# Optimization experiments

Measured on AMD Instinct MI355X. Metric: run time of the kernel, lower is better.

## Reference

```python
import jax, jax.numpy as jnp
import numpy as np

BLOCK = 64
N_HEADS = 16
HEAD_DIM = 64
HIDDEN = N_HEADS * HEAD_DIM
W_BLOCKS = 3   # sliding window blocks (centered: i-1, i, i+1)
G_BLOCKS = 1   # global blocks (block 0)
LN_EPS = 1e-12
NEG = -1e9


def _build_layout(nblk):
    """Static bigbird-style block layout: per query block, indices of attended key blocks.
    Returns idx [nblk, G+W] int32 and valid [nblk, G+W] bool (dedup'd, range-checked)."""
    nkb = G_BLOCKS + W_BLOCKS
    idx = np.zeros((nblk, nkb), dtype=np.int32)
    valid = np.zeros((nblk, nkb), dtype=bool)
    globals_ = list(range(G_BLOCKS))
    half = W_BLOCKS // 2
    for i in range(nblk):
        cands = globals_ + [i - half + j for j in range(W_BLOCKS)]
        seen = set()
        for c, cand in enumerate(cands):
            ok = (0 <= cand < nblk) and (cand not in seen)
            if ok:
                seen.add(cand)
            idx[i, c] = min(max(cand, 0), nblk - 1)
            valid[i, c] = ok
    return jnp.asarray(idx), jnp.asarray(valid)


def setup_inputs() -> dict:
    key = jax.random.key(0)
    ks = jax.random.split(key, 8)
    b, s = 4, 4096
    sd = 1.0 / np.sqrt(HIDDEN)
    inp = {
        "hidden_states": jax.random.normal(ks[0], (b, s, HIDDEN), dtype=jnp.float32),
        "attention_mask": jnp.zeros((b, s), dtype=jnp.float32),
        "wq": jax.random.normal(ks[1], (HIDDEN, HIDDEN), dtype=jnp.float32) * sd,
        "bq": jnp.zeros((HIDDEN,), dtype=jnp.float32),
        "wk": jax.random.normal(ks[2], (HIDDEN, HIDDEN), dtype=jnp.float32) * sd,
        "bk": jnp.zeros((HIDDEN,), dtype=jnp.float32),
        "wv": jax.random.normal(ks[3], (HIDDEN, HIDDEN), dtype=jnp.float32) * sd,
        "bv": jnp.zeros((HIDDEN,), dtype=jnp.float32),
        "wo": jax.random.normal(ks[4], (HIDDEN, HIDDEN), dtype=jnp.float32) * sd,
        "bo": jnp.zeros((HIDDEN,), dtype=jnp.float32),
        "ln_g": jnp.ones((HIDDEN,), dtype=jnp.float32),
        "ln_b": jnp.zeros((HIDDEN,), dtype=jnp.float32),
    }
    return inp


def _sparse_attention(hidden_states, attention_mask, wq, bq, wk, bk, wv, bv, wo, bo, ln_g, ln_b):
    b, s, h = hidden_states.shape
    nblk = s // BLOCK
    idx, valid = _build_layout(nblk)          # [nblk, nkb]
    nkb = idx.shape[1]

    def proj(w, bias):
        y = hidden_states @ w.T + bias                      # [b, s, H]
        return y.reshape(b, s, N_HEADS, HEAD_DIM).transpose(0, 2, 1, 3)  # [b, h, s, d]

    q = proj(wq, bq)
    k = proj(wk, bk)
    v = proj(wv, bv)

    # blockify: [b, h, nblk, BLOCK, d]
    qb = q.reshape(b, N_HEADS, nblk, BLOCK, HEAD_DIM)
    kb = k.reshape(b, N_HEADS, nblk, BLOCK, HEAD_DIM)
    vb = v.reshape(b, N_HEADS, nblk, BLOCK, HEAD_DIM)

    # gather attended key/value blocks per query block: [b, h, nblk, nkb, BLOCK, d]
    kg = kb[:, :, idx]
    vg = vb[:, :, idx]

    scale = 1.0 / np.sqrt(HEAD_DIM)
    # scores: [b, h, nblk, BLOCK(q), nkb, BLOCK(k)]
    scores = jnp.einsum("bhnqd,bhnmkd->bhnqmk", qb, kg) * scale

    # key padding mask (additive float), gathered to sparse layout
    kp = attention_mask.reshape(b, nblk, BLOCK)[:, idx]      # [b, nblk, nkb, BLOCK]
    scores = scores + kp[:, None, :, None, :, :]
    # invalid (out-of-layout) blocks
    scores = jnp.where(valid[None, None, :, None, :, None], scores, NEG)

    # softmax over all attended keys (nkb * BLOCK)
    flat = scores.reshape(b, N_HEADS, nblk, BLOCK, nkb * BLOCK)
    probs = jax.nn.softmax(flat, axis=-1).reshape(scores.shape)

    ctx = jnp.einsum("bhnqmk,bhnmkd->bhnqd", probs, vg)      # [b, h, nblk, BLOCK, d]
    ctx = ctx.reshape(b, N_HEADS, s, HEAD_DIM).transpose(0, 2, 1, 3).reshape(b, s, h)

    # output projection + residual + LayerNorm (dropout in eval mode = identity)
    y = ctx @ wo.T + bo + hidden_states
    mu = jnp.mean(y, axis=-1, keepdims=True)
    var = jnp.mean((y - mu) ** 2, axis=-1, keepdims=True)
    return (y - mu) * jax.lax.rsqrt(var + LN_EPS) * ln_g + ln_b


def reference(hidden_states, attention_mask, wq, bq, wk, bk, wv, bv, wo, bo, ln_g, ln_b):
    return _sparse_attention(hidden_states, attention_mask, wq, bq, wk, bk, wv, bv, wo, bo, ln_g, ln_b)
```

## Files before the change

kernel.cpp:

```cpp
#include <hip/hip_runtime.h>
#include <cstdint>
#include <cstddef>


using f32x4 = __attribute__((ext_vector_type(4))) float;
using s16x8 = __attribute__((ext_vector_type(8))) short;
using u16x4 = __attribute__((ext_vector_type(4))) unsigned short;

#define NEGV -1000000000.0f

__device__ __forceinline__ unsigned short f2b(float f) {
  unsigned u = __float_as_uint(f);
  u += 0x7FFFu + ((u >> 16) & 1u);
  return (unsigned short)(u >> 16);
}

#define GLDS(g, l)                                                        \
  __builtin_amdgcn_global_load_lds(                                       \
      (__attribute__((address_space(1))) void*)(g),                       \
      (__attribute__((address_space(3))) void*)(l), 16, 0, 0)

__global__ __launch_bounds__(256) void cast_hidden(const float* __restrict__ in,
                                                   unsigned short* __restrict__ out) {
  size_t i = (size_t)blockIdx.x * 256 + threadIdx.x;
  float4 v = ((const float4*)in)[i];
  u16x4 o = {f2b(v.x), f2b(v.y), f2b(v.z), f2b(v.w)};
  ((u16x4*)out)[i] = o;
}

__global__ __launch_bounds__(256) void cast_weights(const float* __restrict__ w0,
                                                    const float* __restrict__ w1,
                                                    const float* __restrict__ w2,
                                                    const float* __restrict__ w3,
                                                    unsigned short* __restrict__ out) {
  const float* src = blockIdx.y == 0 ? w0 : blockIdx.y == 1 ? w1 : blockIdx.y == 2 ? w2 : w3;
  size_t i = (size_t)blockIdx.x * 256 + threadIdx.x;
  float4 v = ((const float4*)src)[i];
  u16x4 o = {f2b(v.x), f2b(v.y), f2b(v.z), f2b(v.w)};
  ((u16x4*)(out + (size_t)blockIdx.y * 1048576))[i] = o;
}

template <int MODE>
__global__ __launch_bounds__(256) void gemm128(const unsigned short* __restrict__ A,
                                               const unsigned short* __restrict__ B,
                                               const float* __restrict__ bias,
                                               const float* __restrict__ resid,
                                               void* __restrict__ outp) {
  __shared__ __align__(16) unsigned short As[4096];
  __shared__ __align__(16) unsigned short Bs[4096];
  const int t = threadIdx.x;
  const int wave = t >> 6, lane = t & 63;
  const int quad = lane >> 4, lr = lane & 15;
  const int wm = (wave >> 1) << 6, wn = (wave & 1) << 6;
  const int bm = blockIdx.x << 7, bn = blockIdx.y << 7;

  f32x4 acc[4][4] = {};

  const int srow = t >> 2;
  const int sq = (t & 3) ^ ((srow >> 1) & 3);
  const char* Ag = (const char*)A + (((size_t)(bm + srow)) << 11) + (sq << 4);
  const char* Bg = (const char*)B + (((size_t)(bn + srow)) << 11) + (sq << 4);
  char* AsW = (char*)As + (t << 4);
  char* BsW = (char*)Bs + (t << 4);

  for (int kt = 0; kt < 2048; kt += 64) {
    __syncthreads();
    GLDS(Ag + kt, AsW);
    GLDS(Ag + kt + (64ll << 11), AsW + 4096);
    GLDS(Bg + kt, BsW);
    GLDS(Bg + kt + (64ll << 11), BsW + 4096);
    __syncthreads();
    s16x8 af[4], bf[4];
#pragma unroll
    for (int i = 0; i < 4; ++i) {
      const int ra = wm + i * 16 + lr;
      af[i] = *(const s16x8*)((const char*)As + ra * 64 + ((quad ^ ((ra >> 1) & 3)) << 4));
      const int rb = wn + i * 16 + lr;
      bf[i] = *(const s16x8*)((const char*)Bs + rb * 64 + ((quad ^ ((rb >> 1) & 3)) << 4));
    }
#pragma unroll
    for (int i = 0; i < 4; ++i)
#pragma unroll
      for (int j = 0; j < 4; ++j)
        acc[i][j] = __builtin_amdgcn_mfma_f32_16x16x32_bf16(af[i], bf[j], acc[i][j], 0, 0, 0);
  }

  float bv[4];
#pragma unroll
  for (int j = 0; j < 4; ++j) bv[j] = bias[bn + wn + j * 16 + lr];

  if (MODE == 0) {
    unsigned short* o = (unsigned short*)outp;
    int hh[4], dd[4];
#pragma unroll
    for (int j = 0; j < 4; ++j) {
      int n = bn + wn + j * 16 + lr;
      hh[j] = n >> 6;
      dd[j] = n & 63;
    }
#pragma unroll
    for (int i = 0; i < 4; ++i) {
#pragma unroll
      for (int r = 0; r < 4; ++r) {
        int m = bm + wm + i * 16 + quad * 4 + r;
        int bb = m >> 12, sl = m & 4095;
        size_t base = ((size_t)bb * 16) * 262144 + (size_t)sl * 64;
#pragma unroll
        for (int j = 0; j < 4; ++j)
          o[base + (size_t)hh[j] * 262144 + dd[j]] = f2b(acc[i][j][r] + bv[j]);
      }
    }
  } else {
    float* o = (float*)outp;
#pragma unroll
    for (int i = 0; i < 4; ++i) {
#pragma unroll
      for (int r = 0; r < 4; ++r) {
        size_t m = bm + wm + i * 16 + quad * 4 + r;
        const float* rr = resid + m * 1024 + bn + wn;
        float* orow = o + m * 1024 + bn + wn;
#pragma unroll
        for (int j = 0; j < 4; ++j)
          orow[j * 16 + lr] = acc[i][j][r] + bv[j] + rr[j * 16 + lr];
      }
    }
  }
}

__global__ __launch_bounds__(256) void attn(const unsigned short* __restrict__ Q,
                                            const unsigned short* __restrict__ K,
                                            const unsigned short* __restrict__ V,
                                            const float* __restrict__ amask,
                                            unsigned short* __restrict__ ctx) {
  __shared__ __align__(16) char smem[70656];
  char* Qs = smem;
  char* Ks = smem + 9216;
  char* Pb = smem;
  char* Vt = smem + 33792;
  float* maskL = (float*)(smem + 67584);
  float* wmaxL = (float*)(smem + 68608);
  float* wsumL = (float*)(smem + 69632);

  const int qi = blockIdx.x, h = blockIdx.y, b = blockIdx.z;
  const int t = threadIdx.x;
  const int wave = t >> 6, lane = t & 63;
  const int quad = lane >> 4, lr = lane & 15;

  int kb[4], kv[4];
  kb[0] = 0; kv[0] = 1;
#pragma unroll
  for (int c = 1; c < 4; ++c) {
    int cand = qi - 2 + c;
    kv[c] = (cand >= 1 && cand < 64);
    kb[c] = cand < 0 ? 0 : (cand > 63 ? 63 : cand);
  }

  const size_t bh = ((size_t)b * 16 + h) * 262144;
  const unsigned short* Qg = Q + bh + (size_t)qi * 4096;

  {
    int row = t >> 3, ch = t & 7;
    *(s16x8*)(Qs + row * 144 + ch * 16) = *(const s16x8*)((const char*)Qg + row * 128 + ch * 16);
    *(s16x8*)(Qs + (row + 32) * 144 + ch * 16) =
        *(const s16x8*)((const char*)Qg + (row + 32) * 128 + ch * 16);
#pragma unroll
    for (int c = 0; c < 4; ++c) {
      const unsigned short* Kg = K + bh + (size_t)kb[c] * 4096;
      char* Kc = Ks + c * 9216;
      *(s16x8*)(Kc + row * 144 + ch * 16) = *(const s16x8*)((const char*)Kg + row * 128 + ch * 16);
      *(s16x8*)(Kc + (row + 32) * 144 + ch * 16) =
          *(const s16x8*)((const char*)Kg + (row + 32) * 128 + ch * 16);
    }
  }
  {
    int c = t >> 6, kk = t & 63;
    float mv = amask[(size_t)b * 4096 + kb[c] * 64 + kk];
    maskL[c * 64 + kk] = kv[c] ? mv : mv + NEGV;
  }
  __syncthreads();

  f32x4 s[4][4] = {};
  const char* Kc = Ks + wave * 9216;
#pragma unroll
  for (int ks = 0; ks < 2; ++ks) {
    s16x8 af[4], bf[4];
#pragma unroll
    for (int i = 0; i < 4; ++i) {
      af[i] = *(const s16x8*)(Qs + (i * 16 + lr) * 144 + ks * 64 + quad * 16);
      bf[i] = *(const s16x8*)(Kc + (i * 16 + lr) * 144 + ks * 64 + quad * 16);
    }
#pragma unroll
    for (int i = 0; i < 4; ++i)
#pragma unroll
      for (int j = 0; j < 4; ++j)
        s[i][j] = __builtin_amdgcn_mfma_f32_16x16x32_bf16(af[i], bf[j], s[i][j], 0, 0, 0);
  }
#pragma unroll
  for (int j = 0; j < 4; ++j) {
    const float mj = maskL[wave * 64 + j * 16 + lr];
#pragma unroll
    for (int i = 0; i < 4; ++i)
#pragma unroll
      for (int r = 0; r < 4; ++r) s[i][j][r] = s[i][j][r] * 0.125f + mj;
  }
  __syncthreads();

#pragma unroll
  for (int i = 0; i < 4; ++i)
#pragma unroll
    for (int r = 0; r < 4; ++r) {
      float m0 = fmaxf(fmaxf(s[i][0][r], s[i][1][r]), fmaxf(s[i][2][r], s[i][3][r]));
      m0 = fmaxf(m0, __shfl_xor(m0, 1, 64));
      m0 = fmaxf(m0, __shfl_xor(m0, 2, 64));
      m0 = fmaxf(m0, __shfl_xor(m0, 4, 64));
      m0 = fmaxf(m0, __shfl_xor(m0, 8, 64));
      if (lr == 0) wmaxL[(i * 16 + quad * 4 + r) * 4 + wave] = m0;
    }

  {
    int kk = t & 63, dc0 = t >> 6;
#pragma unroll
    for (int c = 0; c < 4; ++c) {
      const unsigned short* Vg = V + bh + (size_t)kb[c] * 4096 + (size_t)kk * 64;
#pragma unroll
      for (int rr = 0; rr < 2; ++rr) {
        int dc = dc0 + rr * 4;
        s16x8 vv = *(const s16x8*)(Vg + dc * 8);
#pragma unroll
        for (int e = 0; e < 8; ++e)
          *(unsigned short*)(Vt + (dc * 8 + e) * 528 + (c * 64 + kk) * 2) = vv[e];
      }
    }
  }
  __syncthreads();

#pragma unroll
  for (int i = 0; i < 4; ++i)
#pragma unroll
    for (int r = 0; r < 4; ++r) {
      int row = i * 16 + quad * 4 + r;
      f32x4 wmv = *(const f32x4*)(wmaxL + row * 4);
      float g = fmaxf(fmaxf(wmv[0], wmv[1]), fmaxf(wmv[2], wmv[3]));
      float sm = 0.f;
#pragma unroll
      for (int j = 0; j < 4; ++j) {
        float e = __expf(s[i][j][r] - g);
        s[i][j][r] = e;
        sm += e;
      }
      sm += __shfl_xor(sm, 1, 64);
      sm += __shfl_xor(sm, 2, 64);
      sm += __shfl_xor(sm, 4, 64);
      sm += __shfl_xor(sm, 8, 64);
      if (lr == 0) wsumL[row * 4 + wave] = sm;
    }
#pragma unroll
  for (int i = 0; i < 4; ++i)
#pragma unroll
    for (int r = 0; r < 4; ++r) {
      char* prow = Pb + (i * 16 + quad * 4 + r) * 528 + wave * 128 + lr * 2;
#pragma unroll
      for (int j = 0; j < 4; ++j) *(unsigned short*)(prow + j * 32) = f2b(s[i][j][r]);
    }
  __syncthreads();

  f32x4 acc2[4] = {};
  const char* Prow = Pb + (wave * 16 + lr) * 528;
#pragma unroll
  for (int ks = 0; ks < 8; ++ks) {
    s16x8 a = *(const s16x8*)(Prow + ks * 64 + quad * 16);
#pragma unroll
    for (int j = 0; j < 4; ++j) {
      s16x8 bb2 = *(const s16x8*)(Vt + (j * 16 + lr) * 528 + ks * 64 + quad * 16);
      acc2[j] = __builtin_amdgcn_mfma_f32_16x16x32_bf16(a, bb2, acc2[j], 0, 0, 0);
    }
  }
  float inv[4];
#pragma unroll
  for (int r = 0; r < 4; ++r) {
    int row = wave * 16 + quad * 4 + r;
    f32x4 wsv = *(const f32x4*)(wsumL + row * 4);
    inv[r] = 1.0f / (wsv[0] + wsv[1] + wsv[2] + wsv[3]);
  }
#pragma unroll
  for (int r = 0; r < 4; ++r) {
    size_t srow = (size_t)qi * 64 + wave * 16 + quad * 4 + r;
    size_t base = ((size_t)b * 4096 + srow) * 1024 + h * 64;
#pragma unroll
    for (int j = 0; j < 4; ++j) ctx[base + j * 16 + lr] = f2b(acc2[j][r] * inv[r]);
  }
}

__global__ __launch_bounds__(256) void lnorm(float* __restrict__ y,
                                             const float* __restrict__ g,
                                             const float* __restrict__ bta) {
  __shared__ float red[8];
  float4* p = (float4*)(y + (size_t)blockIdx.x * 1024);
  float4 v = p[threadIdx.x];
  float s1 = v.x + v.y + v.z + v.w;
  float s2 = v.x * v.x + v.y * v.y + v.z * v.z + v.w * v.w;
#pragma unroll
  for (int m = 1; m <= 32; m <<= 1) {
    s1 += __shfl_xor(s1, m, 64);
    s2 += __shfl_xor(s2, m, 64);
  }
  int wv = threadIdx.x >> 6;
  if ((threadIdx.x & 63) == 0) {
    red[wv] = s1;
    red[4 + wv] = s2;
  }
  __syncthreads();
  float t1 = red[0] + red[1] + red[2] + red[3];
  float t2 = red[4] + red[5] + red[6] + red[7];
  float mu = t1 * (1.0f / 1024.0f);
  float var = t2 * (1.0f / 1024.0f) - mu * mu;
  float rs = rsqrtf(var + 1e-12f);
  float4 gg = ((const float4*)g)[threadIdx.x];
  float4 bb = ((const float4*)bta)[threadIdx.x];
  float4 o;
  o.x = (v.x - mu) * rs * gg.x + bb.x;
  o.y = (v.y - mu) * rs * gg.y + bb.y;
  o.z = (v.z - mu) * rs * gg.z + bb.z;
  o.w = (v.w - mu) * rs * gg.w + bb.w;
  p[threadIdx.x] = o;
}

extern "C" void kernel_launch(void* const* d_in, const int* in_sizes, int n_in,
                              void* d_out, int out_size, void* d_ws, size_t ws_size,
                              hipStream_t stream) {
  (void)in_sizes; (void)n_in; (void)out_size; (void)ws_size;
  const float* hs = (const float*)d_in[0];
  const float* amask = (const float*)d_in[1];
  const float* wq = (const float*)d_in[2];
  const float* bq = (const float*)d_in[3];
  const float* wk = (const float*)d_in[4];
  const float* bk = (const float*)d_in[5];
  const float* wv = (const float*)d_in[6];
  const float* bv = (const float*)d_in[7];
  const float* wo = (const float*)d_in[8];
  const float* bo = (const float*)d_in[9];
  const float* lg = (const float*)d_in[10];
  const float* lb = (const float*)d_in[11];

  char* ws = (char*)d_ws;
  unsigned short* hbf = (unsigned short*)(ws);
  unsigned short* wqb = (unsigned short*)(ws + 33554432);
  unsigned short* qb  = (unsigned short*)(ws + 41943040);
  unsigned short* kbb = (unsigned short*)(ws + 75497472);
  unsigned short* vbb = (unsigned short*)(ws + 109051904);
  unsigned short* cxb = (unsigned short*)(ws + 142606336);
  unsigned short* wkb = wqb + 1048576;
  unsigned short* wvb = wkb + 1048576;
  unsigned short* wob = wvb + 1048576;
  float* out = (float*)d_out;

  cast_hidden<<<16384, 256, 0, stream>>>(hs, hbf);
  cast_weights<<<dim3(1024, 4), 256, 0, stream>>>(wq, wk, wv, wo, wqb);

  dim3 gg(128, 8);
  gemm128<0><<<gg, 256, 0, stream>>>(hbf, wqb, bq, nullptr, qb);
  gemm128<0><<<gg, 256, 0, stream>>>(hbf, wkb, bk, nullptr, kbb);
  gemm128<0><<<gg, 256, 0, stream>>>(hbf, wvb, bv, nullptr, vbb);

  attn<<<dim3(64, 16, 4), 256, 0, stream>>>(qb, kbb, vbb, amask, cxb);

  gemm128<1><<<gg, 256, 0, stream>>>(cxb, wob, bo, hs, (void*)out);
  lnorm<<<16384, 256, 0, stream>>>(out, lg, lb);
}
```

Measured before the change: 461.7 us.

## Emit V transposed from projection GEMM and simplify attention LDS staging

After: 462.7 us. About the same (+0.2%).

```diff
diff --git a/kernel.cpp b/kernel.cpp
--- a/kernel.cpp
+++ b/kernel.cpp
@@ -110,6 +110,28 @@
           o[base + (size_t)hh[j] * 262144 + dd[j]] = f2b(acc[i][j][r] + bv[j]);
       }
     }
+  } else if (MODE == 2) {
+    unsigned short* o = (unsigned short*)outp;
+    int hh[4], dd[4];
+#pragma unroll
+    for (int j = 0; j < 4; ++j) {
+      int n = bn + wn + j * 16 + lr;
+      hh[j] = n >> 6;
+      dd[j] = n & 63;
+    }
+#pragma unroll
+    for (int i = 0; i < 4; ++i) {
+#pragma unroll
+      for (int r = 0; r < 4; ++r) {
+        int m = bm + wm + i * 16 + quad * 4 + r;
+        int bb = m >> 12, blk = (m >> 6) & 63, mi = m & 63;
+        int sg = (mi & 15) * 4 + (mi >> 4);
+#pragma unroll
+        for (int j = 0; j < 4; ++j)
+          o[(((size_t)bb * 16 + hh[j]) * 64 + dd[j]) * 4096 + blk * 64 + sg] =
+              f2b(acc[i][j][r] + bv[j]);
+      }
+    }
   } else {
     float* o = (float*)outp;
 #pragma unroll
@@ -129,17 +151,16 @@
 
 __global__ __launch_bounds__(256) void attn(const unsigned short* __restrict__ Q,
                                             const unsigned short* __restrict__ K,
-                                            const unsigned short* __restrict__ V,
+                                            const unsigned short* __restrict__ vT,
                                             const float* __restrict__ amask,
                                             unsigned short* __restrict__ ctx) {
-  __shared__ __align__(16) char smem[70656];
+  __shared__ __align__(16) char smem[69632];
   char* Qs = smem;
   char* Ks = smem + 9216;
   char* Pb = smem;
   char* Vt = smem + 33792;
-  float* maskL = (float*)(smem + 67584);
-  float* wmaxL = (float*)(smem + 68608);
-  float* wsumL = (float*)(smem + 69632);
+  float* wmaxL = (float*)(smem + 67584);
+  float* wsumL = (float*)(smem + 68608);
 
   const int qi = blockIdx.x, h = blockIdx.y, b = blockIdx.z;
   const int t = threadIdx.x;
@@ -172,10 +193,11 @@
           *(const s16x8*)((const char*)Kg + (row + 32) * 128 + ch * 16);
     }
   }
-  {
-    int c = t >> 6, kk = t & 63;
-    float mv = amask[(size_t)b * 4096 + kb[c] * 64 + kk];
-    maskL[c * 64 + kk] = kv[c] ? mv : mv + NEGV;
+  float mj[4];
+#pragma unroll
+  for (int j = 0; j < 4; ++j) {
+    float mv = amask[(size_t)b * 4096 + kb[wave] * 64 + j * 16 + lr];
+    mj[j] = kv[wave] ? mv : mv + NEGV;
   }
   __syncthreads();
 
@@ -196,15 +218,11 @@
         s[i][j] = __builtin_amdgcn_mfma_f32_16x16x32_bf16(af[i], bf[j], s[i][j], 0, 0, 0);
   }
 #pragma unroll
-  for (int j = 0; j < 4; ++j) {
-    const float mj = maskL[wave * 64 + j * 16 + lr];
+  for (int j = 0; j < 4; ++j)
 #pragma unroll
     for (int i = 0; i < 4; ++i)
 #pragma unroll
-      for (int r = 0; r < 4; ++r) s[i][j][r] = s[i][j][r] * 0.125f + mj;
-  }
-  __syncthreads();
-
+      for (int r = 0; r < 4; ++r) s[i][j][r] = s[i][j][r] * 0.125f + mj[j];
 #pragma unroll
   for (int i = 0; i < 4; ++i)
 #pragma unroll
@@ -216,23 +234,16 @@
       m0 = fmaxf(m0, __shfl_xor(m0, 8, 64));
       if (lr == 0) wmaxL[(i * 16 + quad * 4 + r) * 4 + wave] = m0;
     }
+  __syncthreads();
 
   {
-    int kk = t & 63, dc0 = t >> 6;
-#pragma unroll
-    for (int c = 0; c < 4; ++c) {
-      const unsigned short* Vg = V + bh + (size_t)kb[c] * 4096 + (size_t)kk * 64;
-#pragma unroll
-      for (int rr = 0; rr < 2; ++rr) {
-        int dc = dc0 + rr * 4;
-        s16x8 vv = *(const s16x8*)(Vg + dc * 8);
-#pragma unroll
-        for (int e = 0; e < 8; ++e)
-          *(unsigned short*)(Vt + (dc * 8 + e) * 528 + (c * 64 + kk) * 2) = vv[e];
-      }
-    }
-  }
-  __syncthreads();
+    int d = t & 63;
+    const unsigned short* src = vT + (((size_t)b * 16 + h) * 64 + d) * 4096 + kb[wave] * 64;
+    char* dst = Vt + d * 528 + wave * 128;
+#pragma unroll
+    for (int ch = 0; ch < 8; ++ch)
+      *(s16x8*)(dst + ch * 16) = *(const s16x8*)((const char*)src + ch * 16);
+  }
 
 #pragma unroll
   for (int i = 0; i < 4; ++i)
@@ -241,26 +252,18 @@
       int row = i * 16 + quad * 4 + r;
       f32x4 wmv = *(const f32x4*)(wmaxL + row * 4);
       float g = fmaxf(fmaxf(wmv[0], wmv[1]), fmaxf(wmv[2], wmv[3]));
-      float sm = 0.f;
-#pragma unroll
-      for (int j = 0; j < 4; ++j) {
-        float e = __expf(s[i][j][r] - g);
-        s[i][j][r] = e;
-        sm += e;
-      }
+      float e0 = __expf(s[i][0][r] - g);
+      float e1 = __expf(s[i][1][r] - g);
+      float e2 = __expf(s[i][2][r] - g);
+      float e3 = __expf(s[i][3][r] - g);
+      float sm = (e0 + e1) + (e2 + e3);
       sm += __shfl_xor(sm, 1, 64);
       sm += __shfl_xor(sm, 2, 64);
       sm += __shfl_xor(sm, 4, 64);
       sm += __shfl_xor(sm, 8, 64);
       if (lr == 0) wsumL[row * 4 + wave] = sm;
-    }
-#pragma unroll
-  for (int i = 0; i < 4; ++i)
-#pragma unroll
-    for (int r = 0; r < 4; ++r) {
-      char* prow = Pb + (i * 16 + quad * 4 + r) * 528 + wave * 128 + lr * 2;
-#pragma unroll
-      for (int j = 0; j < 4; ++j) *(unsigned short*)(prow + j * 32) = f2b(s[i][j][r]);
+      u16x4 pv = {f2b(e0), f2b(e1), f2b(e2), f2b(e3)};
+      *(u16x4*)(Pb + row * 528 + wave * 128 + lr * 8) = pv;
     }
   __syncthreads();
 
@@ -347,7 +350,7 @@
   unsigned short* wqb = (unsigned short*)(ws + 33554432);
   unsigned short* qb  = (unsigned short*)(ws + 41943040);
   unsigned short* kbb = (unsigned short*)(ws + 75497472);
-  unsigned short* vbb = (unsigned short*)(ws + 109051904);
+  unsigned short* vtb = (unsigned short*)(ws + 109051904);
   unsigned short* cxb = (unsigned short*)(ws + 142606336);
   unsigned short* wkb = wqb + 1048576;
   unsigned short* wvb = wkb + 1048576;
@@ -360,9 +363,9 @@
   dim3 gg(128, 8);
   gemm128<0><<<gg, 256, 0, stream>>>(hbf, wqb, bq, nullptr, qb);
   gemm128<0><<<gg, 256, 0, stream>>>(hbf, wkb, bk, nullptr, kbb);
-  gemm128<0><<<gg, 256, 0, stream>>>(hbf, wvb, bv, nullptr, vbb);
-
-  attn<<<dim3(64, 16, 4), 256, 0, stream>>>(qb, kbb, vbb, amask, cxb);
+  gemm128<2><<<gg, 256, 0, stream>>>(hbf, wvb, bv, nullptr, vtb);
+
+  attn<<<dim3(64, 16, 4), 256, 0, stream>>>(qb, kbb, vtb, amask, cxb);
 
   gemm128<1><<<gg, 256, 0, stream>>>(cxb, wob, bo, hs, (void*)out);
   lnorm<<<16384, 256, 0, stream>>>(out, lg, lb);
```
